# Kernel optimization log

Hardware: AMD Instinct MI355X
Metric: run time of the kernel (lower is better)

Reference implementation:

```python
import jax, jax.numpy as jnp
import numpy as np

N_NODES = 4096
N_HEADS = 8
NEG_SLOPE = 0.2  # PyG GATConv default leaky_relu slope


def _gat_single(h, src, dst, att_src, att_dst):
    # h: [N, H, C] projected node features; src/dst: [E] (self-loops included)
    a_s = (h * att_src).sum(-1)                      # [N, H]
    a_d = (h * att_dst).sum(-1)                      # [N, H]
    e = jax.nn.leaky_relu(a_s[src] + a_d[dst], NEG_SLOPE)   # [E, H]
    m = jax.ops.segment_max(e, dst, num_segments=N_NODES)   # [N, H]
    ex = jnp.exp(e - m[dst])                         # [E, H]
    denom = jax.ops.segment_sum(ex, dst, num_segments=N_NODES)
    alpha = ex / denom[dst]                          # [E, H] (self-loops => denom > 0)
    out = jax.ops.segment_sum(alpha[:, :, None] * h[src], dst, num_segments=N_NODES)
    return out                                       # [N, H, C]


def setup_inputs() -> dict:
    key = jax.random.key(0)
    ks = jax.random.split(key, 12)
    B, T, N, F = 4, 12, N_NODES, 8
    Hg, Hl = 64, 128
    inp = {
        "x": jax.random.normal(ks[0], (B, T, N, F), jnp.float32),
        "edge_index": jax.random.randint(ks[1], (2, 65536), 0, N, jnp.int64),
        "W_gat": jax.random.normal(ks[2], (F, Hg), jnp.float32) * 0.3,
        "att_src": jax.random.normal(ks[3], (N_HEADS, Hg // N_HEADS), jnp.float32) * 0.3,
        "att_dst": jax.random.normal(ks[4], (N_HEADS, Hg // N_HEADS), jnp.float32) * 0.3,
        "b_gat": jax.random.normal(ks[5], (Hg,), jnp.float32) * 0.1,
        "W_ih": jax.random.normal(ks[6], (4 * Hl, Hg * N), jnp.float32) * 0.002,
        "W_hh": jax.random.normal(ks[7], (4 * Hl, Hl), jnp.float32) * 0.05,
        "b_ih": jax.random.normal(ks[8], (4 * Hl,), jnp.float32) * 0.05,
        "b_hh": jax.random.normal(ks[9], (4 * Hl,), jnp.float32) * 0.05,
        "W_fc": jax.random.normal(ks[10], (Hl, N * F), jnp.float32) * 0.05,
        "b_fc": jax.random.normal(ks[11], (N * F,), jnp.float32) * 0.05,
    }
    return inp


def reference(x, edge_index, W_gat, att_src, att_dst, b_gat,
              W_ih, W_hh, b_ih, b_hh, W_fc, b_fc):
    B, T, N, F = x.shape
    H = N_HEADS
    C = W_gat.shape[1] // H
    Hl = W_hh.shape[1]

    # add self-loops (PyG GATConv default add_self_loops=True)
    loop = jnp.arange(N, dtype=edge_index.dtype)
    src = jnp.concatenate([edge_index[0], loop])
    dst = jnp.concatenate([edge_index[1], loop])

    # ---- GAT over all (batch, time) graphs at once ----
    h = (x.reshape(B * T, N, F) @ W_gat).reshape(B * T, N, H, C)
    gat = jax.vmap(_gat_single, in_axes=(0, None, None, None, None))(
        h, src, dst, att_src, att_dst)                # [BT, N, H, C]
    gat = gat.reshape(B * T, N, H * C) + b_gat
    gat = jax.nn.elu(gat)                             # dropout p=0 (eval) => identity
    seq = gat.reshape(B, T, N * H * C)

    # ---- LSTM (torch gate order: i, f, g, o) ----
    def step(carry, x_t):
        hprev, cprev = carry
        gates = x_t @ W_ih.T + b_ih + hprev @ W_hh.T + b_hh   # [B, 4Hl]
        i, f, g, o = jnp.split(gates, 4, axis=-1)
        c = jax.nn.sigmoid(f) * cprev + jax.nn.sigmoid(i) * jnp.tanh(g)
        hn = jax.nn.sigmoid(o) * jnp.tanh(c)
        return (hn, c), None

    h0 = jnp.zeros((B, Hl), x.dtype)
    (h_last, _), _ = jax.lax.scan(step, (h0, h0), seq.transpose(1, 0, 2))

    out = h_last @ W_fc + b_fc
    return out.reshape(B, N, F)
```

## Files before the change

### kernel.cpp

```cpp
#include <hip/hip_runtime.h>

#define NN 4096
#define NH 8
#define BTT 48
#define KG 262144
#define NJ 512
#define HLL 128
#define ERAW 65536
#define NKC 256

typedef __attribute__((ext_vector_type(8))) short bf16x8;
typedef __attribute__((ext_vector_type(4))) float f32x4;
typedef __attribute__((ext_vector_type(8))) unsigned short ushort8;

typedef __attribute__((address_space(1))) const void* as1_cvp;
typedef __attribute__((address_space(3))) void* as3_vp;

__device__ __forceinline__ unsigned short f2bf(float f) {
  unsigned int u = __float_as_uint(f);
  u += 0x7FFFu + ((u >> 16) & 1u);
  return (unsigned short)(u >> 16);
}
__device__ __forceinline__ float bf2f(unsigned short s) {
  return __uint_as_float(((unsigned int)s) << 16);
}

__global__ __launch_bounds__(256) void k_init(int* __restrict__ counts) {
  int t = blockIdx.x * 256 + threadIdx.x;
  counts[t] = 1;
}

__global__ __launch_bounds__(256) void k_hist(const int* __restrict__ ei, int* __restrict__ counts) {
  int e = blockIdx.x * 256 + threadIdx.x;
  atomicAdd(&counts[ei[ERAW + e]], 1);
}

__global__ __launch_bounds__(1024) void k_scan(const int* __restrict__ counts, int* __restrict__ offs,
                                               int* __restrict__ cursor, int* __restrict__ ssrc) {
  __shared__ int p[1024];
  int t = threadIdx.x;
  int i0 = t * 4;
  int c0 = counts[i0], c1 = counts[i0 + 1], c2 = counts[i0 + 2], c3 = counts[i0 + 3];
  int s = c0 + c1 + c2 + c3;
  p[t] = s;
  __syncthreads();
  for (int off = 1; off < 1024; off <<= 1) {
    int v = (t >= off) ? p[t - off] : 0;
    __syncthreads();
    p[t] += v;
    __syncthreads();
  }
  int base = p[t] - s;
  int o0 = base, o1 = o0 + c0, o2 = o1 + c1, o3 = o2 + c2;
  offs[i0] = o0; offs[i0 + 1] = o1; offs[i0 + 2] = o2; offs[i0 + 3] = o3;
  if (t == 1023) offs[NN] = o3 + c3;
  cursor[i0] = o0 + 1; cursor[i0 + 1] = o1 + 1; cursor[i0 + 2] = o2 + 1; cursor[i0 + 3] = o3 + 1;
  ssrc[o0] = i0; ssrc[o1] = i0 + 1; ssrc[o2] = i0 + 2; ssrc[o3] = i0 + 3;
}

__global__ __launch_bounds__(256) void k_scatter(const int* __restrict__ ei, int* __restrict__ cursor,
                                                 int* __restrict__ ssrc) {
  int e = blockIdx.x * 256 + threadIdx.x;
  int s = ei[e], d = ei[ERAW + e];
  int pos = atomicAdd(&cursor[d], 1);
  ssrc[pos] = s;
}

__global__ __launch_bounds__(256) void k_proj(const float* __restrict__ x, const float* __restrict__ Wg,
                                              const float* __restrict__ att_s, const float* __restrict__ att_d,
                                              unsigned short* __restrict__ h, float* __restrict__ a_s,
                                              float* __restrict__ a_d) {
  __shared__ float wgs[512];
  __shared__ float ats[64], atd[64];
  int tid = threadIdx.x;
  wgs[tid] = Wg[tid];
  wgs[256 + tid] = Wg[256 + tid];
  if (tid < 64) { ats[tid] = att_s[tid]; atd[tid] = att_d[tid]; }
  __syncthreads();
  int bt = blockIdx.x >> 7;
  int inner = blockIdx.x & 127;
  int hd = tid & 7, nl = tid >> 3;
  int n = inner * 32 + nl;
  const float* xr = x + ((size_t)(bt * NN + n)) * 8;
  float4 xa = *(const float4*)xr, xb2 = *(const float4*)(xr + 4);
  float xv[8] = {xa.x, xa.y, xa.z, xa.w, xb2.x, xb2.y, xb2.z, xb2.w};
  int hb = hd * 8;
  float hv[8];
#pragma unroll
  for (int c = 0; c < 8; ++c) {
    float acc = 0.f;
#pragma unroll
    for (int f = 0; f < 8; ++f) acc += xv[f] * wgs[f * 64 + hb + c];
    hv[c] = acc;
  }
  float as = 0.f, ad = 0.f;
#pragma unroll
  for (int c = 0; c < 8; ++c) { as += hv[c] * ats[hb + c]; ad += hv[c] * atd[hb + c]; }
  int aoff = bt * (NN * NH) + n * NH + hd;
  a_s[aoff] = as;
  a_d[aoff] = ad;
  ushort8 hr;
#pragma unroll
  for (int c = 0; c < 8; ++c) hr[c] = f2bf(hv[c]);
  *(ushort8*)(h + (size_t)bt * KG + (size_t)n * 64 + hb) = hr;
}

__global__ __launch_bounds__(256) void k_gat(const unsigned short* __restrict__ h, const float* __restrict__ a_s,
                                             const float* __restrict__ a_d, const int* __restrict__ offs,
                                             const int* __restrict__ ssrc, const float* __restrict__ b_gat,
                                             unsigned short* __restrict__ Xb) {
  int bt = blockIdx.x >> 7;
  int inner = blockIdx.x & 127;
  int tid = threadIdx.x;
  int hd = tid & 7, nl = tid >> 3;
  int n = inner * 32 + nl;
  const unsigned short* hbase = h + (size_t)bt * KG;
  const float* asb = a_s + bt * (NN * NH);
  float adn = a_d[bt * (NN * NH) + n * NH + hd];
  int beg = offs[n], end = offs[n + 1];
  float m = -INFINITY, ssum = 0.f;
  float o[8];
#pragma unroll
  for (int c = 0; c < 8; ++c) o[c] = 0.f;
  for (int i = beg; i < end; ++i) {
    int s = ssrc[i];
    float e = asb[s * NH + hd] + adn;
    e = (e > 0.f) ? e : 0.2f * e;
    if (e > m) {
      float r = __expf(m - e);
      ssum *= r;
#pragma unroll
      for (int c = 0; c < 8; ++c) o[c] *= r;
      m = e;
    }
    float p = __expf(e - m);
    ssum += p;
    ushort8 hvv = *(const ushort8*)(hbase + (size_t)s * 64 + hd * 8);
#pragma unroll
    for (int c = 0; c < 8; ++c) o[c] += p * bf2f(hvv[c]);
  }
  float inv = 1.f / ssum;
  ushort8 r;
#pragma unroll
  for (int c = 0; c < 8; ++c) {
    float v = o[c] * inv + b_gat[hd * 8 + c];
    v = (v > 0.f) ? v : (__expf(v) - 1.f);
    r[c] = f2bf(v);
  }
  *(ushort8*)(Xb + (size_t)bt * KG + (size_t)n * 64 + hd * 8) = r;
}

__global__ __launch_bounds__(256) void k_gemm(const unsigned short* __restrict__ Xb,
                                              const float* __restrict__ Wih, float* __restrict__ Gp) {
  __shared__ float Wt[2][4096];
  int tid = threadIdx.x;
  int w = tid >> 6, lane = tid & 63;
  int lm = lane & 15, kg = lane >> 4;
  int jb = blockIdx.x & 3;
  int kc = blockIdx.x >> 2;
  int j0 = jb * 128;
  size_t kbase = (size_t)kc * 1024;

  const float* sbase[4];
#pragma unroll
  for (int i = 0; i < 4; ++i) {
    int row = ((w * 4 + i) << 3) + (lane >> 3);
    int colf = ((lane & 7) ^ (row & 7)) << 2;
    sbase[i] = Wih + (size_t)(j0 + row) * KG + kbase + colf;
  }

  f32x4 acc[3][2];
#pragma unroll
  for (int mf = 0; mf < 3; ++mf)
#pragma unroll
    for (int jf = 0; jf < 2; ++jf) acc[mf][jf] = f32x4{0.f, 0.f, 0.f, 0.f};

#pragma unroll
  for (int i = 0; i < 4; ++i)
    __builtin_amdgcn_global_load_lds((as1_cvp)(sbase[i]),
                                     (as3_vp)((char*)&Wt[0][0] + (w * 4 + i) * 1024), 16, 0, 0);
  __syncthreads();

  const short* Xs = (const short*)Xb;
  int cur = 0;
  for (int t = 0; t < 32; ++t) {
    size_t k = kbase + (size_t)t * 32 + kg * 8;
    bf16x8 a0 = *(const bf16x8*)(Xs + (size_t)lm * KG + k);
    bf16x8 a1 = *(const bf16x8*)(Xs + (size_t)(16 + lm) * KG + k);
    bf16x8 a2 = *(const bf16x8*)(Xs + (size_t)(32 + lm) * KG + k);
    if (t + 1 < 32) {
      int off = (t + 1) * 32;
#pragma unroll
      for (int i = 0; i < 4; ++i)
        __builtin_amdgcn_global_load_lds((as1_cvp)(sbase[i] + off),
                                         (as3_vp)((char*)&Wt[cur ^ 1][0] + (w * 4 + i) * 1024), 16, 0, 0);
    }
    const char* tile = (const char*)&Wt[cur][0];
#pragma unroll
    for (int jf = 0; jf < 2; ++jf) {
      int row = w * 32 + jf * 16 + lm;
      int A0 = row * 128 + ((kg * 32) ^ ((row & 7) << 4));
      float4 f0 = *(const float4*)(tile + A0);
      float4 f1 = *(const float4*)(tile + (A0 ^ 16));
      bf16x8 b;
      b[0] = (short)f2bf(f0.x); b[1] = (short)f2bf(f0.y);
      b[2] = (short)f2bf(f0.z); b[3] = (short)f2bf(f0.w);
      b[4] = (short)f2bf(f1.x); b[5] = (short)f2bf(f1.y);
      b[6] = (short)f2bf(f1.z); b[7] = (short)f2bf(f1.w);
      acc[0][jf] = __builtin_amdgcn_mfma_f32_16x16x32_bf16(a0, b, acc[0][jf], 0, 0, 0);
      acc[1][jf] = __builtin_amdgcn_mfma_f32_16x16x32_bf16(a1, b, acc[1][jf], 0, 0, 0);
      acc[2][jf] = __builtin_amdgcn_mfma_f32_16x16x32_bf16(a2, b, acc[2][jf], 0, 0, 0);
    }
    __syncthreads();
    cur ^= 1;
  }

  float* gout = Gp + (size_t)kc * (BTT * NJ);
#pragma unroll
  for (int mf = 0; mf < 3; ++mf)
#pragma unroll
    for (int jf = 0; jf < 2; ++jf) {
      int j = j0 + w * 32 + jf * 16 + lm;
#pragma unroll
      for (int r = 0; r < 4; ++r) {
        int bt = mf * 16 + kg * 4 + r;
        gout[bt * NJ + j] = acc[mf][jf][r];
      }
    }
}

__global__ __launch_bounds__(256) void k_red(const float* __restrict__ Gp, float* __restrict__ G) {
  int gid = blockIdx.x * 256 + threadIdx.x;
  float acc = 0.f;
#pragma unroll 4
  for (int kc = 0; kc < NKC; ++kc) acc += Gp[(size_t)kc * (BTT * NJ) + gid];
  G[gid] = acc;
}

__global__ __launch_bounds__(512) void k_lstm(const float* __restrict__ G, const float* __restrict__ Whh,
                                              const float* __restrict__ bih, const float* __restrict__ bhh,
                                              float* __restrict__ hlast) {
  __shared__ float hs[HLL];
  __shared__ float gs[NJ];
  int b = blockIdx.x, j = threadIdx.x;
  float bias = bih[j] + bhh[j];
  float w[HLL];
  const float* wr = Whh + (size_t)j * HLL;
#pragma unroll
  for (int k = 0; k < HLL; k += 4) {
    float4 v = *(const float4*)(wr + k);
    w[k] = v.x; w[k + 1] = v.y; w[k + 2] = v.z; w[k + 3] = v.w;
  }
  if (j < HLL) hs[j] = 0.f;
  float c = 0.f;
  __syncthreads();
  for (int t = 0; t < 12; ++t) {
    const float* g0 = G + (size_t)(b * 12 + t) * NJ;
    float acc = g0[j] + bias;
#pragma unroll
    for (int k = 0; k < HLL; ++k) acc += w[k] * hs[k];
    gs[j] = acc;
    __syncthreads();
    if (j < HLL) {
      float gi = gs[j], gf = gs[HLL + j], gg = gs[2 * HLL + j], go = gs[3 * HLL + j];
      float si = 1.f / (1.f + __expf(-gi));
      float sf = 1.f / (1.f + __expf(-gf));
      float so = 1.f / (1.f + __expf(-go));
      c = sf * c + si * tanhf(gg);
      hs[j] = so * tanhf(c);
    }
    __syncthreads();
  }
  if (j < HLL) hlast[b * HLL + j] = hs[j];
}

__global__ __launch_bounds__(256) void k_fc(const float* __restrict__ hlast, const float* __restrict__ Wfc,
                                            const float* __restrict__ bfc, float* __restrict__ out) {
  __shared__ float hl[NJ];
  int tid = threadIdx.x;
  hl[tid] = hlast[tid];
  hl[256 + tid] = hlast[256 + tid];
  __syncthreads();
  int n = blockIdx.x * 256 + tid;
  float a0 = 0.f, a1 = 0.f, a2 = 0.f, a3 = 0.f;
  for (int k = 0; k < HLL; ++k) {
    float wv = Wfc[(size_t)k * 32768 + n];
    a0 += hl[k] * wv;
    a1 += hl[HLL + k] * wv;
    a2 += hl[2 * HLL + k] * wv;
    a3 += hl[3 * HLL + k] * wv;
  }
  float bb = bfc[n];
  out[n] = a0 + bb;
  out[32768 + n] = a1 + bb;
  out[65536 + n] = a2 + bb;
  out[98304 + n] = a3 + bb;
}

extern "C" void kernel_launch(void* const* d_in, const int* in_sizes, int n_in,
                              void* d_out, int out_size, void* d_ws, size_t ws_size,
                              hipStream_t stream) {
  const float* x     = (const float*)d_in[0];
  const int*   ei    = (const int*)d_in[1];
  const float* Wg    = (const float*)d_in[2];
  const float* att_s = (const float*)d_in[3];
  const float* att_d = (const float*)d_in[4];
  const float* b_gat = (const float*)d_in[5];
  const float* Wih   = (const float*)d_in[6];
  const float* Whh   = (const float*)d_in[7];
  const float* bih   = (const float*)d_in[8];
  const float* bhh   = (const float*)d_in[9];
  const float* Wfc   = (const float*)d_in[10];
  const float* bfc   = (const float*)d_in[11];
  float* out = (float*)d_out;

  char* ws = (char*)d_ws;
  unsigned short* h  = (unsigned short*)(ws);
  float* a_s         = (float*)(ws + 25165824);
  float* a_d         = (float*)(ws + 31457280);
  unsigned short* Xb = (unsigned short*)(ws + 37748736);
  float* Gp          = (float*)(ws + 62914560);
  float* G           = (float*)(ws + 88080384);
  float* hlast       = (float*)(ws + 88178688);
  int* counts        = (int*)(ws + 88180736);
  int* offs          = (int*)(ws + 88197120);
  int* cursor        = (int*)(ws + 88213760);
  int* ssrc          = (int*)(ws + 88230144);

  hipLaunchKernelGGL(k_init,    dim3(16),       dim3(256),  0, stream, counts);
  hipLaunchKernelGGL(k_hist,    dim3(256),      dim3(256),  0, stream, ei, counts);
  hipLaunchKernelGGL(k_scan,    dim3(1),        dim3(1024), 0, stream, counts, offs, cursor, ssrc);
  hipLaunchKernelGGL(k_scatter, dim3(256),      dim3(256),  0, stream, ei, cursor, ssrc);
  hipLaunchKernelGGL(k_proj,    dim3(48 * 128), dim3(256),  0, stream, x, Wg, att_s, att_d, h, a_s, a_d);
  hipLaunchKernelGGL(k_gat,     dim3(48 * 128), dim3(256),  0, stream, h, a_s, a_d, offs, ssrc, b_gat, Xb);
  hipLaunchKernelGGL(k_gemm,    dim3(1024),     dim3(256),  0, stream, Xb, Wih, Gp);
  hipLaunchKernelGGL(k_red,     dim3(96),       dim3(256),  0, stream, Gp, G);
  hipLaunchKernelGGL(k_lstm,    dim3(4),        dim3(512),  0, stream, G, Whh, bih, bhh, hlast);
  hipLaunchKernelGGL(k_fc,      dim3(128),      dim3(256),  0, stream, hlast, Wfc, bfc, out);
}
```

Before: 341.3 us.

## Load W_ih tiles directly into registers and split partial-sum reduction into two stages

The GEMM kernel no longer stages W_ih through LDS with global_load_lds and barriers. Each lane now loads its own float4 slices straight into registers, double-buffered alongside the activation fragments, which removes the per-iteration __syncthreads. The single k_red pass, which ran only 96 blocks each looping over 256 partials, becomes a 768-block first stage that sums 32 partials per slot followed by a small second stage. This gains parallelism in the reduction and drops the barrier overhead, at the cost of an extra launch, an extra intermediate buffer, and possibly less coalesced direct global loads in the GEMM.

After: 331.6 us. -2.9%, faster.

```diff
diff --git a/kernel.cpp b/kernel.cpp
--- a/kernel.cpp
+++ b/kernel.cpp
@@ -8,13 +8,11 @@
 #define HLL 128
 #define ERAW 65536
 #define NKC 256
+#define NG  24576
 
 typedef __attribute__((ext_vector_type(8))) short bf16x8;
 typedef __attribute__((ext_vector_type(4))) float f32x4;
 typedef __attribute__((ext_vector_type(8))) unsigned short ushort8;
-
-typedef __attribute__((address_space(1))) const void* as1_cvp;
-typedef __attribute__((address_space(3))) void* as3_vp;
 
 __device__ __forceinline__ unsigned short f2bf(float f) {
   unsigned int u = __float_as_uint(f);
@@ -152,22 +150,20 @@
 
 __global__ __launch_bounds__(256) void k_gemm(const unsigned short* __restrict__ Xb,
                                               const float* __restrict__ Wih, float* __restrict__ Gp) {
-  __shared__ float Wt[2][4096];
   int tid = threadIdx.x;
   int w = tid >> 6, lane = tid & 63;
   int lm = lane & 15, kg = lane >> 4;
   int jb = blockIdx.x & 3;
   int kc = blockIdx.x >> 2;
-  int j0 = jb * 128;
-  size_t kbase = (size_t)kc * 1024;
-
-  const float* sbase[4];
-#pragma unroll
-  for (int i = 0; i < 4; ++i) {
-    int row = ((w * 4 + i) << 3) + (lane >> 3);
-    int colf = ((lane & 7) ^ (row & 7)) << 2;
-    sbase[i] = Wih + (size_t)(j0 + row) * KG + kbase + colf;
-  }
+  int j0 = jb * 128 + w * 32;
+  size_t kbase = (size_t)kc * 1024 + kg * 8;
+
+  const float* wr0 = Wih + (size_t)(j0 + lm) * KG + kbase;
+  const float* wr1 = Wih + (size_t)(j0 + 16 + lm) * KG + kbase;
+  const short* Xs = (const short*)Xb;
+  const short* xr0 = Xs + (size_t)lm * KG + kbase;
+  const short* xr1 = xr0 + (size_t)16 * KG;
+  const short* xr2 = xr0 + (size_t)32 * KG;
 
   f32x4 acc[3][2];
 #pragma unroll
@@ -175,52 +171,50 @@
 #pragma unroll
     for (int jf = 0; jf < 2; ++jf) acc[mf][jf] = f32x4{0.f, 0.f, 0.f, 0.f};
 
-#pragma unroll
-  for (int i = 0; i < 4; ++i)
-    __builtin_amdgcn_global_load_lds((as1_cvp)(sbase[i]),
-                                     (as3_vp)((char*)&Wt[0][0] + (w * 4 + i) * 1024), 16, 0, 0);
-  __syncthreads();
-
-  const short* Xs = (const short*)Xb;
-  int cur = 0;
+  float4 wbuf[2][4];
+  bf16x8 abuf[2][3];
+
+  wbuf[0][0] = *(const float4*)(wr0);
+  wbuf[0][1] = *(const float4*)(wr0 + 4);
+  wbuf[0][2] = *(const float4*)(wr1);
+  wbuf[0][3] = *(const float4*)(wr1 + 4);
+  abuf[0][0] = *(const bf16x8*)(xr0);
+  abuf[0][1] = *(const bf16x8*)(xr1);
+  abuf[0][2] = *(const bf16x8*)(xr2);
+
+#pragma unroll 2
   for (int t = 0; t < 32; ++t) {
-    size_t k = kbase + (size_t)t * 32 + kg * 8;
-    bf16x8 a0 = *(const bf16x8*)(Xs + (size_t)lm * KG + k);
-    bf16x8 a1 = *(const bf16x8*)(Xs + (size_t)(16 + lm) * KG + k);
-    bf16x8 a2 = *(const bf16x8*)(Xs + (size_t)(32 + lm) * KG + k);
+    int cur = t & 1, nxt = cur ^ 1;
     if (t + 1 < 32) {
       int off = (t + 1) * 32;
-#pragma unroll
-      for (int i = 0; i < 4; ++i)
-        __builtin_amdgcn_global_load_lds((as1_cvp)(sbase[i] + off),
-                                         (as3_vp)((char*)&Wt[cur ^ 1][0] + (w * 4 + i) * 1024), 16, 0, 0);
-    }
-    const char* tile = (const char*)&Wt[cur][0];
+      wbuf[nxt][0] = *(const float4*)(wr0 + off);
+      wbuf[nxt][1] = *(const float4*)(wr0 + off + 4);
+      wbuf[nxt][2] = *(const float4*)(wr1 + off);
+      wbuf[nxt][3] = *(const float4*)(wr1 + off + 4);
+      abuf[nxt][0] = *(const bf16x8*)(xr0 + off);
+      abuf[nxt][1] = *(const bf16x8*)(xr1 + off);
+      abuf[nxt][2] = *(const bf16x8*)(xr2 + off);
+    }
 #pragma unroll
     for (int jf = 0; jf < 2; ++jf) {
-      int row = w * 32 + jf * 16 + lm;
-      int A0 = row * 128 + ((kg * 32) ^ ((row & 7) << 4));
-      float4 f0 = *(const float4*)(tile + A0);
-      float4 f1 = *(const float4*)(tile + (A0 ^ 16));
+      float4 f0 = wbuf[cur][jf * 2], f1 = wbuf[cur][jf * 2 + 1];
       bf16x8 b;
       b[0] = (short)f2bf(f0.x); b[1] = (short)f2bf(f0.y);
       b[2] = (short)f2bf(f0.z); b[3] = (short)f2bf(f0.w);
       b[4] = (short)f2bf(f1.x); b[5] = (short)f2bf(f1.y);
       b[6] = (short)f2bf(f1.z); b[7] = (short)f2bf(f1.w);
-      acc[0][jf] = __builtin_amdgcn_mfma_f32_16x16x32_bf16(a0, b, acc[0][jf], 0, 0, 0);
-      acc[1][jf] = __builtin_amdgcn_mfma_f32_16x16x32_bf16(a1, b, acc[1][jf], 0, 0, 0);
-      acc[2][jf] = __builtin_amdgcn_mfma_f32_16x16x32_bf16(a2, b, acc[2][jf], 0, 0, 0);
-    }
-    __syncthreads();
-    cur ^= 1;
-  }
-
-  float* gout = Gp + (size_t)kc * (BTT * NJ);
+      acc[0][jf] = __builtin_amdgcn_mfma_f32_16x16x32_bf16(abuf[cur][0], b, acc[0][jf], 0, 0, 0);
+      acc[1][jf] = __builtin_amdgcn_mfma_f32_16x16x32_bf16(abuf[cur][1], b, acc[1][jf], 0, 0, 0);
+      acc[2][jf] = __builtin_amdgcn_mfma_f32_16x16x32_bf16(abuf[cur][2], b, acc[2][jf], 0, 0, 0);
+    }
+  }
+
+  float* gout = Gp + (size_t)kc * NG;
 #pragma unroll
   for (int mf = 0; mf < 3; ++mf)
 #pragma unroll
     for (int jf = 0; jf < 2; ++jf) {
-      int j = j0 + w * 32 + jf * 16 + lm;
+      int j = j0 + jf * 16 + lm;
 #pragma unroll
       for (int r = 0; r < 4; ++r) {
         int bt = mf * 16 + kg * 4 + r;
@@ -229,11 +223,23 @@
     }
 }
 
-__global__ __launch_bounds__(256) void k_red(const float* __restrict__ Gp, float* __restrict__ G) {
+__global__ __launch_bounds__(256) void k_red1(const float* __restrict__ Gp, float* __restrict__ Gp2) {
+  int idx = blockIdx.x * 256 + threadIdx.x;
+  int seg = idx >> 14;
+  seg = idx / NG;
+  int gid = idx - seg * NG;
+  const float* src = Gp + (size_t)seg * 32 * NG + gid;
+  float acc = 0.f;
+#pragma unroll 8
+  for (int i = 0; i < 32; ++i) acc += src[(size_t)i * NG];
+  Gp2[idx] = acc;
+}
+
+__global__ __launch_bounds__(256) void k_red2(const float* __restrict__ Gp2, float* __restrict__ G) {
   int gid = blockIdx.x * 256 + threadIdx.x;
   float acc = 0.f;
-#pragma unroll 4
-  for (int kc = 0; kc < NKC; ++kc) acc += Gp[(size_t)kc * (BTT * NJ) + gid];
+#pragma unroll
+  for (int s = 0; s < 8; ++s) acc += Gp2[s * NG + gid];
   G[gid] = acc;
 }
 
@@ -326,6 +332,7 @@
   int* offs          = (int*)(ws + 88197120);
   int* cursor        = (int*)(ws + 88213760);
   int* ssrc          = (int*)(ws + 88230144);
+  float* Gp2         = (float*)(ws + 88508672);
 
   hipLaunchKernelGGL(k_init,    dim3(16),       dim3(256),  0, stream, counts);
   hipLaunchKernelGGL(k_hist,    dim3(256),      dim3(256),  0, stream, ei, counts);
@@ -334,7 +341,8 @@
   hipLaunchKernelGGL(k_proj,    dim3(48 * 128), dim3(256),  0, stream, x, Wg, att_s, att_d, h, a_s, a_d);
   hipLaunchKernelGGL(k_gat,     dim3(48 * 128), dim3(256),  0, stream, h, a_s, a_d, offs, ssrc, b_gat, Xb);
   hipLaunchKernelGGL(k_gemm,    dim3(1024),     dim3(256),  0, stream, Xb, Wih, Gp);
-  hipLaunchKernelGGL(k_red,     dim3(96),       dim3(256),  0, stream, Gp, G);
+  hipLaunchKernelGGL(k_red1,    dim3(768),      dim3(256),  0, stream, Gp, Gp2);
+  hipLaunchKernelGGL(k_red2,    dim3(96),       dim3(256),  0, stream, Gp2, G);
   hipLaunchKernelGGL(k_lstm,    dim3(4),        dim3(512),  0, stream, G, Whh, bih, bhh, hlast);
   hipLaunchKernelGGL(k_fc,      dim3(128),      dim3(256),  0, stream, hlast, Wfc, bfc, out);
 }
```

## Triple-buffer GEMM weight tiles, fuse CSR build, split-K reduction across stages

Applied to the files above, without the earlier changes.

The input-projection GEMM moves from a double-buffered loop with a __syncthreads every step to a three-slot software pipeline. It uses only per-wave vmcnt waits and sched barriers, which works because each wave consumes only the weight rows it loaded itself. The four CSR-building kernels are merged into one single-block kernel that counts and scatters with LDS atomics, cutting launch overhead and global atomics. The 256-way split-K reduction, which ran on only 96 blocks, becomes a 768-block first stage of 32-way partial sums, and the last 8-way sum is folded into the LSTM kernel. The risks are the hand-tuned waitcnt counts being wrong and a serial single-block CSR kernel.

After: 457.9 us. +34.2%, slower.

```diff
diff --git a/kernel.cpp b/kernel.cpp
--- a/kernel.cpp
+++ b/kernel.cpp
@@ -8,6 +8,7 @@
 #define HLL 128
 #define ERAW 65536
 #define NKC 256
+#define NG  24576
 
 typedef __attribute__((ext_vector_type(8))) short bf16x8;
 typedef __attribute__((ext_vector_type(4))) float f32x4;
@@ -25,45 +26,38 @@
   return __uint_as_float(((unsigned int)s) << 16);
 }
 
-__global__ __launch_bounds__(256) void k_init(int* __restrict__ counts) {
-  int t = blockIdx.x * 256 + threadIdx.x;
-  counts[t] = 1;
-}
-
-__global__ __launch_bounds__(256) void k_hist(const int* __restrict__ ei, int* __restrict__ counts) {
-  int e = blockIdx.x * 256 + threadIdx.x;
-  atomicAdd(&counts[ei[ERAW + e]], 1);
-}
-
-__global__ __launch_bounds__(1024) void k_scan(const int* __restrict__ counts, int* __restrict__ offs,
-                                               int* __restrict__ cursor, int* __restrict__ ssrc) {
-  __shared__ int p[1024];
+__global__ __launch_bounds__(1024) void k_csr(const int* __restrict__ ei, int* __restrict__ offs,
+                                              int* __restrict__ ssrc) {
+  __shared__ int cnt[NN];
+  __shared__ int ps[1024];
   int t = threadIdx.x;
+  for (int i = t; i < NN; i += 1024) cnt[i] = 1;
+  __syncthreads();
+  for (int e = t; e < ERAW; e += 1024) atomicAdd(&cnt[ei[ERAW + e]], 1);
+  __syncthreads();
   int i0 = t * 4;
-  int c0 = counts[i0], c1 = counts[i0 + 1], c2 = counts[i0 + 2], c3 = counts[i0 + 3];
+  int c0 = cnt[i0], c1 = cnt[i0 + 1], c2 = cnt[i0 + 2], c3 = cnt[i0 + 3];
   int s = c0 + c1 + c2 + c3;
-  p[t] = s;
+  ps[t] = s;
   __syncthreads();
   for (int off = 1; off < 1024; off <<= 1) {
-    int v = (t >= off) ? p[t - off] : 0;
+    int v = (t >= off) ? ps[t - off] : 0;
     __syncthreads();
-    p[t] += v;
+    ps[t] += v;
     __syncthreads();
   }
-  int base = p[t] - s;
+  int base = ps[t] - s;
   int o0 = base, o1 = o0 + c0, o2 = o1 + c1, o3 = o2 + c2;
   offs[i0] = o0; offs[i0 + 1] = o1; offs[i0 + 2] = o2; offs[i0 + 3] = o3;
   if (t == 1023) offs[NN] = o3 + c3;
-  cursor[i0] = o0 + 1; cursor[i0 + 1] = o1 + 1; cursor[i0 + 2] = o2 + 1; cursor[i0 + 3] = o3 + 1;
+  cnt[i0] = o0 + 1; cnt[i0 + 1] = o1 + 1; cnt[i0 + 2] = o2 + 1; cnt[i0 + 3] = o3 + 1;
   ssrc[o0] = i0; ssrc[o1] = i0 + 1; ssrc[o2] = i0 + 2; ssrc[o3] = i0 + 3;
-}
-
-__global__ __launch_bounds__(256) void k_scatter(const int* __restrict__ ei, int* __restrict__ cursor,
-                                                 int* __restrict__ ssrc) {
-  int e = blockIdx.x * 256 + threadIdx.x;
-  int s = ei[e], d = ei[ERAW + e];
-  int pos = atomicAdd(&cursor[d], 1);
-  ssrc[pos] = s;
+  __syncthreads();
+  for (int e = t; e < ERAW; e += 1024) {
+    int s2 = ei[e], d = ei[ERAW + e];
+    int pos = atomicAdd(&cnt[d], 1);
+    ssrc[pos] = s2;
+  }
 }
 
 __global__ __launch_bounds__(256) void k_proj(const float* __restrict__ x, const float* __restrict__ Wg,
@@ -150,15 +144,47 @@
   *(ushort8*)(Xb + (size_t)bt * KG + (size_t)n * 64 + hd * 8) = r;
 }
 
+#define WAITVM(n) asm volatile("s_waitcnt vmcnt(" #n ")" ::: "memory")
+
+#define GRP(sl, tt) do {                                                          \
+    int off_ = (tt) * 32;                                                         \
+    xb_[sl][0] = *(const bf16x8*)(xr0 + off_);                                    \
+    xb_[sl][1] = *(const bf16x8*)(xr1 + off_);                                    \
+    xb_[sl][2] = *(const bf16x8*)(xr2 + off_);                                    \
+    _Pragma("unroll")                                                             \
+    for (int i_ = 0; i_ < 4; ++i_)                                                \
+      __builtin_amdgcn_global_load_lds((as1_cvp)(sbase[i_] + off_),               \
+          (as3_vp)(wlds + (sl) * 16384 + (w * 4 + i_) * 1024), 16, 0, 0);         \
+  } while (0)
+
+#define CONS(sl) do {                                                             \
+    const char* tile_ = wlds + (sl) * 16384;                                      \
+    _Pragma("unroll")                                                             \
+    for (int jf = 0; jf < 2; ++jf) {                                              \
+      int row_ = w * 32 + jf * 16 + lm;                                           \
+      int A0_ = row_ * 128 + ((kg * 32) ^ ((row_ & 7) << 4));                     \
+      float4 f0 = *(const float4*)(tile_ + A0_);                                  \
+      float4 f1 = *(const float4*)(tile_ + (A0_ ^ 16));                           \
+      bf16x8 bfr;                                                                 \
+      bfr[0] = (short)f2bf(f0.x); bfr[1] = (short)f2bf(f0.y);                     \
+      bfr[2] = (short)f2bf(f0.z); bfr[3] = (short)f2bf(f0.w);                     \
+      bfr[4] = (short)f2bf(f1.x); bfr[5] = (short)f2bf(f1.y);                     \
+      bfr[6] = (short)f2bf(f1.z); bfr[7] = (short)f2bf(f1.w);                     \
+      acc[0][jf] = __builtin_amdgcn_mfma_f32_16x16x32_bf16(xb_[sl][0], bfr, acc[0][jf], 0, 0, 0); \
+      acc[1][jf] = __builtin_amdgcn_mfma_f32_16x16x32_bf16(xb_[sl][1], bfr, acc[1][jf], 0, 0, 0); \
+      acc[2][jf] = __builtin_amdgcn_mfma_f32_16x16x32_bf16(xb_[sl][2], bfr, acc[2][jf], 0, 0, 0); \
+    }                                                                             \
+  } while (0)
+
 __global__ __launch_bounds__(256) void k_gemm(const unsigned short* __restrict__ Xb,
                                               const float* __restrict__ Wih, float* __restrict__ Gp) {
-  __shared__ float Wt[2][4096];
+  __shared__ float Wt[3][4096];
+  char* wlds = (char*)&Wt[0][0];
   int tid = threadIdx.x;
   int w = tid >> 6, lane = tid & 63;
   int lm = lane & 15, kg = lane >> 4;
   int jb = blockIdx.x & 3;
   int kc = blockIdx.x >> 2;
-  int j0 = jb * 128;
   size_t kbase = (size_t)kc * 1024;
 
   const float* sbase[4];
@@ -166,8 +192,12 @@
   for (int i = 0; i < 4; ++i) {
     int row = ((w * 4 + i) << 3) + (lane >> 3);
     int colf = ((lane & 7) ^ (row & 7)) << 2;
-    sbase[i] = Wih + (size_t)(j0 + row) * KG + kbase + colf;
-  }
+    sbase[i] = Wih + (size_t)(jb * 128 + row) * KG + kbase + colf;
+  }
+  const short* Xs = (const short*)Xb;
+  const short* xr0 = Xs + (size_t)lm * KG + kbase + kg * 8;
+  const short* xr1 = xr0 + (size_t)16 * KG;
+  const short* xr2 = xr0 + (size_t)32 * KG;
 
   f32x4 acc[3][2];
 #pragma unroll
@@ -175,52 +205,24 @@
 #pragma unroll
     for (int jf = 0; jf < 2; ++jf) acc[mf][jf] = f32x4{0.f, 0.f, 0.f, 0.f};
 
-#pragma unroll
-  for (int i = 0; i < 4; ++i)
-    __builtin_amdgcn_global_load_lds((as1_cvp)(sbase[i]),
-                                     (as3_vp)((char*)&Wt[0][0] + (w * 4 + i) * 1024), 16, 0, 0);
-  __syncthreads();
-
-  const short* Xs = (const short*)Xb;
-  int cur = 0;
-  for (int t = 0; t < 32; ++t) {
-    size_t k = kbase + (size_t)t * 32 + kg * 8;
-    bf16x8 a0 = *(const bf16x8*)(Xs + (size_t)lm * KG + k);
-    bf16x8 a1 = *(const bf16x8*)(Xs + (size_t)(16 + lm) * KG + k);
-    bf16x8 a2 = *(const bf16x8*)(Xs + (size_t)(32 + lm) * KG + k);
-    if (t + 1 < 32) {
-      int off = (t + 1) * 32;
-#pragma unroll
-      for (int i = 0; i < 4; ++i)
-        __builtin_amdgcn_global_load_lds((as1_cvp)(sbase[i] + off),
-                                         (as3_vp)((char*)&Wt[cur ^ 1][0] + (w * 4 + i) * 1024), 16, 0, 0);
-    }
-    const char* tile = (const char*)&Wt[cur][0];
+  bf16x8 xb_[3][3];
+
+  GRP(0, 0);
+  GRP(1, 1);
+  for (int tb = 0; tb < 30; tb += 3) {
+    GRP(2, tb + 2); WAITVM(14); __builtin_amdgcn_sched_barrier(0); CONS(0);
+    GRP(0, tb + 3); WAITVM(14); __builtin_amdgcn_sched_barrier(0); CONS(1);
+    GRP(1, tb + 4); WAITVM(14); __builtin_amdgcn_sched_barrier(0); CONS(2);
+  }
+  WAITVM(7);  __builtin_amdgcn_sched_barrier(0); CONS(0);
+  WAITVM(0);  __builtin_amdgcn_sched_barrier(0); CONS(1);
+
+  float* gout = Gp + (size_t)kc * NG;
+#pragma unroll
+  for (int mf = 0; mf < 3; ++mf)
 #pragma unroll
     for (int jf = 0; jf < 2; ++jf) {
-      int row = w * 32 + jf * 16 + lm;
-      int A0 = row * 128 + ((kg * 32) ^ ((row & 7) << 4));
-      float4 f0 = *(const float4*)(tile + A0);
-      float4 f1 = *(const float4*)(tile + (A0 ^ 16));
-      bf16x8 b;
-      b[0] = (short)f2bf(f0.x); b[1] = (short)f2bf(f0.y);
-      b[2] = (short)f2bf(f0.z); b[3] = (short)f2bf(f0.w);
-      b[4] = (short)f2bf(f1.x); b[5] = (short)f2bf(f1.y);
-      b[6] = (short)f2bf(f1.z); b[7] = (short)f2bf(f1.w);
-      acc[0][jf] = __builtin_amdgcn_mfma_f32_16x16x32_bf16(a0, b, acc[0][jf], 0, 0, 0);
-      acc[1][jf] = __builtin_amdgcn_mfma_f32_16x16x32_bf16(a1, b, acc[1][jf], 0, 0, 0);
-      acc[2][jf] = __builtin_amdgcn_mfma_f32_16x16x32_bf16(a2, b, acc[2][jf], 0, 0, 0);
-    }
-    __syncthreads();
-    cur ^= 1;
-  }
-
-  float* gout = Gp + (size_t)kc * (BTT * NJ);
-#pragma unroll
-  for (int mf = 0; mf < 3; ++mf)
-#pragma unroll
-    for (int jf = 0; jf < 2; ++jf) {
-      int j = j0 + w * 32 + jf * 16 + lm;
+      int j = jb * 128 + w * 32 + jf * 16 + lm;
 #pragma unroll
       for (int r = 0; r < 4; ++r) {
         int bt = mf * 16 + kg * 4 + r;
@@ -229,15 +231,18 @@
     }
 }
 
-__global__ __launch_bounds__(256) void k_red(const float* __restrict__ Gp, float* __restrict__ G) {
-  int gid = blockIdx.x * 256 + threadIdx.x;
+__global__ __launch_bounds__(256) void k_red1(const float* __restrict__ Gp, float* __restrict__ Gp2) {
+  int idx = blockIdx.x * 256 + threadIdx.x;
+  int seg = idx / NG;
+  int gid = idx - seg * NG;
+  const float* src = Gp + (size_t)seg * 32 * NG + gid;
   float acc = 0.f;
-#pragma unroll 4
-  for (int kc = 0; kc < NKC; ++kc) acc += Gp[(size_t)kc * (BTT * NJ) + gid];
-  G[gid] = acc;
-}
-
-__global__ __launch_bounds__(512) void k_lstm(const float* __restrict__ G, const float* __restrict__ Whh,
+#pragma unroll 8
+  for (int i = 0; i < 32; ++i) acc += src[(size_t)i * NG];
+  Gp2[idx] = acc;
+}
+
+__global__ __launch_bounds__(512) void k_lstm(const float* __restrict__ Gp2, const float* __restrict__ Whh,
                                               const float* __restrict__ bih, const float* __restrict__ bhh,
                                               float* __restrict__ hlast) {
   __shared__ float hs[HLL];
@@ -255,8 +260,10 @@
   float c = 0.f;
   __syncthreads();
   for (int t = 0; t < 12; ++t) {
-    const float* g0 = G + (size_t)(b * 12 + t) * NJ;
-    float acc = g0[j] + bias;
+    const float* gp = Gp2 + (size_t)(b * 12 + t) * NJ + j;
+    float acc = bias;
+#pragma unroll
+    for (int s = 0; s < 8; ++s) acc += gp[(size_t)s * NG];
 #pragma unroll
     for (int k = 0; k < HLL; ++k) acc += w[k] * hs[k];
     gs[j] = acc;
@@ -283,6 +290,7 @@
   __syncthreads();
   int n = blockIdx.x * 256 + tid;
   float a0 = 0.f, a1 = 0.f, a2 = 0.f, a3 = 0.f;
+#pragma unroll 8
   for (int k = 0; k < HLL; ++k) {
     float wv = Wfc[(size_t)k * 32768 + n];
     a0 += hl[k] * wv;
@@ -320,21 +328,16 @@
   float* a_d         = (float*)(ws + 31457280);
   unsigned short* Xb = (unsigned short*)(ws + 37748736);
   float* Gp          = (float*)(ws + 62914560);
-  float* G           = (float*)(ws + 88080384);
-  float* hlast       = (float*)(ws + 88178688);
-  int* counts        = (int*)(ws + 88180736);
-  int* offs          = (int*)(ws + 88197120);
-  int* cursor        = (int*)(ws + 88213760);
-  int* ssrc          = (int*)(ws + 88230144);
-
-  hipLaunchKernelGGL(k_init,    dim3(16),       dim3(256),  0, stream, counts);
-  hipLaunchKernelGGL(k_hist,    dim3(256),      dim3(256),  0, stream, ei, counts);
-  hipLaunchKernelGGL(k_scan,    dim3(1),        dim3(1024), 0, stream, counts, offs, cursor, ssrc);
-  hipLaunchKernelGGL(k_scatter, dim3(256),      dim3(256),  0, stream, ei, cursor, ssrc);
-  hipLaunchKernelGGL(k_proj,    dim3(48 * 128), dim3(256),  0, stream, x, Wg, att_s, att_d, h, a_s, a_d);
-  hipLaunchKernelGGL(k_gat,     dim3(48 * 128), dim3(256),  0, stream, h, a_s, a_d, offs, ssrc, b_gat, Xb);
-  hipLaunchKernelGGL(k_gemm,    dim3(1024),     dim3(256),  0, stream, Xb, Wih, Gp);
-  hipLaunchKernelGGL(k_red,     dim3(96),       dim3(256),  0, stream, Gp, G);
-  hipLaunchKernelGGL(k_lstm,    dim3(4),        dim3(512),  0, stream, G, Whh, bih, bhh, hlast);
-  hipLaunchKernelGGL(k_fc,      dim3(128),      dim3(256),  0, stream, hlast, Wfc, bfc, out);
-}
+  float* Gp2         = (float*)(ws + 88080384);
+  float* hlast       = (float*)(ws + 88866816);
+  int* offs          = (int*)(ws + 88868864);
+  int* ssrc          = (int*)(ws + 88885256);
+
+  hipLaunchKernelGGL(k_csr,  dim3(1),        dim3(1024), 0, stream, ei, offs, ssrc);
+  hipLaunchKernelGGL(k_proj, dim3(48 * 128), dim3(256),  0, stream, x, Wg, att_s, att_d, h, a_s, a_d);
+  hipLaunchKernelGGL(k_gat,  dim3(48 * 128), dim3(256),  0, stream, h, a_s, a_d, offs, ssrc, b_gat, Xb);
+  hipLaunchKernelGGL(k_gemm, dim3(1024),     dim3(256),  0, stream, Xb, Wih, Gp);
+  hipLaunchKernelGGL(k_red1, dim3(768),      dim3(256),  0, stream, Gp, Gp2);
+  hipLaunchKernelGGL(k_lstm, dim3(4),        dim3(512),  0, stream, Gp2, Whh, bih, bhh, hlast);
+  hipLaunchKernelGGL(k_fc,   dim3(128),      dim3(256),  0, stream, hlast, Wfc, bfc, out);
+}
```
